# Optimization experiments

Hardware: AMD Instinct MI355X
Metric: run time of the kernel (lower is better)

The kernel has to match this reference:

```python
import jax, jax.numpy as jnp
import numpy as np


def setup_inputs() -> dict:
    key = jax.random.key(0)
    ks = jax.random.split(key, 9)
    B, Nq, Nkv, C, ICO = 1, 512, 2562, 64, 64
    return {
        "q": jax.random.normal(ks[0], (B, Nq, C), jnp.float32),
        "q_coord": jax.random.normal(ks[1], (B, Nq, 3), jnp.float32),
        "kv": jax.random.normal(ks[2], (B, Nkv, ICO), jnp.float32),
        "kv_coord": jax.random.normal(ks[3], (B, Nkv, 3), jnp.float32),
        "Wq": jax.random.normal(ks[4], (C, C), jnp.float32) * (C ** -0.5),
        "Wkv": jax.random.normal(ks[5], (ICO, 2 * C), jnp.float32) * (ICO ** -0.5),
        "Wdelta": jax.random.normal(ks[6], (3, C), jnp.float32) * (3 ** -0.5),
        "Wproj": jax.random.normal(ks[7], (C, C), jnp.float32) * (C ** -0.5),
        "bproj": jnp.zeros((C,), jnp.float32),
    }


def reference(q, q_coord, kv, kv_coord, Wq, Wkv, Wdelta, Wproj, bproj):
    C = q.shape[-1]
    scale = 1.0 / C  # erp_dim ** -1 (qk_scale=None)
    q_ = q @ Wq                                   # [B, Nq, C]
    kv_ = kv @ Wkv                                # [B, Nkv, 2C]
    k, v = jnp.split(kv_, 2, axis=-1)             # each [B, Nkv, C]
    # positional encoding: exp(-|dq - dk|) over 3D coords, projected to C
    pos_enc = jnp.exp(-jnp.abs(q_coord[:, :, None] - kv_coord[:, None])) @ Wdelta  # [B,Nq,Nkv,C]
    # elementwise abs-diff attention score, reduced over channel dim
    score = (jnp.exp(-jnp.abs(q_[:, :, None] - k[:, None])) + pos_enc).sum(-1) * scale  # [B,Nq,Nkv]
    attn = jax.nn.softmax(score, axis=-1)
    out = attn @ v                                # [B, Nq, C]
    return out @ Wproj + bproj
```

## Files before the change

kernel.cpp:

```cpp
#include <hip/hip_runtime.h>

#define NQ   512
#define NKV  2562
#define CH   64
#define QB   4
#define BT   256
#define NJQ  8
#define JQ   321
#define PSTRIDE 260
#define LOG2E 1.44269504088896340736f

#define KVROWS 8
#define NKVB ((NKV + KVROWS - 1) / KVROWS)
#define QROWS 16
#define NQB (NQ / QROWS)
#define NCB  41

static __device__ __forceinline__ float exp2_raw(float x) {
  float r; asm("v_exp_f32 %0, %1" : "=v"(r) : "v"(x)); return r;
}
static __device__ __forceinline__ float exp2_negabs(float x) {
  float r; asm("v_exp_f32 %0, -abs(%1)" : "=v"(r) : "v"(x)); return r;
}
#define E2(a, b) exp2_negabs((a) - (b))
#define T4(qf, kf) ((E2((qf).x, (kf).x) + E2((qf).y, (kf).y)) + \
                    (E2((qf).z, (kf).z) + E2((qf).w, (kf).w)))

__global__ __launch_bounds__(256) void gemm_qkv(
    const float* __restrict__ q, const float* __restrict__ kv,
    const float* __restrict__ Wq, const float* __restrict__ Wkv,
    const float* __restrict__ kvc, float* __restrict__ qp,
    float* __restrict__ kvp, float* __restrict__ kvc4) {
  const int tid = threadIdx.x;
  if (blockIdx.x < NKVB) {
    const int j0 = blockIdx.x * KVROWS;
    __shared__ float s_in[KVROWS][CH];
    if (tid < KVROWS * (CH / 4)) {
      int r = tid >> 4, g = tid & 15;
      int j = j0 + r;
      float4 v = (j < NKV) ? ((const float4*)(kv + (size_t)j * CH))[g]
                           : make_float4(0.f, 0.f, 0.f, 0.f);
      ((float4*)&s_in[r][0])[g] = v;
    }
    __syncthreads();
    const int r = tid >> 5;
    const int mg = (tid & 31) * 4;
    float4 acc = make_float4(0.f, 0.f, 0.f, 0.f);
#pragma unroll 16
    for (int rr = 0; rr < CH; ++rr) {
      float a = s_in[r][rr];
      float4 w = *(const float4*)(Wkv + (size_t)rr * 2 * CH + mg);
      acc.x = fmaf(a, w.x, acc.x); acc.y = fmaf(a, w.y, acc.y);
      acc.z = fmaf(a, w.z, acc.z); acc.w = fmaf(a, w.w, acc.w);
    }
    if (mg < CH) {
      acc.x *= LOG2E; acc.y *= LOG2E; acc.z *= LOG2E; acc.w *= LOG2E;
    }
    int j = j0 + r;
    if (j < NKV) *(float4*)(kvp + (size_t)j * 2 * CH + mg) = acc;
  } else if (blockIdx.x < NKVB + NQB) {
    const int i0 = (blockIdx.x - NKVB) * QROWS;
    __shared__ float s_in[QROWS][CH];
    {
      int r = tid >> 4, g = tid & 15;
      float4 v = ((const float4*)(q + (size_t)(i0 + r) * CH))[g];
      ((float4*)&s_in[r][0])[g] = v;
    }
    __syncthreads();
    const int r = tid >> 4;
    const int cg = (tid & 15) * 4;
    float4 acc = make_float4(0.f, 0.f, 0.f, 0.f);
#pragma unroll 16
    for (int rr = 0; rr < CH; ++rr) {
      float a = s_in[r][rr];
      float4 w = *(const float4*)(Wq + (size_t)rr * CH + cg);
      acc.x = fmaf(a, w.x, acc.x); acc.y = fmaf(a, w.y, acc.y);
      acc.z = fmaf(a, w.z, acc.z); acc.w = fmaf(a, w.w, acc.w);
    }
    acc.x *= LOG2E; acc.y *= LOG2E; acc.z *= LOG2E; acc.w *= LOG2E;
    *(float4*)(qp + (size_t)(i0 + r) * CH + cg) = acc;
  } else {
    int t = (blockIdx.x - NKVB - NQB) * 256 + tid;
    if (t < NKV * 4) {
      int j = t >> 2, d = t & 3;
      kvc4[t] = (d < 3) ? kvc[(size_t)j * 3 + d] * LOG2E : 0.f;
    }
  }
}

__global__ __launch_bounds__(BT, 4) void attn_part(
    const float* __restrict__ qp, const float* __restrict__ kvp,
    const float* __restrict__ qc, const float* __restrict__ kvc4,
    const float* __restrict__ Wdelta, float* __restrict__ part) {
  __shared__ float s_score[QB][JQ];
  __shared__ float s_red[QB][BT];
  __shared__ float s_wd[3];

  const int qquad = blockIdx.x >> 3;
  const int h = blockIdx.x & 7;
  const int i0 = qquad * QB;
  const int jlo = h * JQ;
  const int jhi = (jlo + JQ < NKV) ? jlo + JQ : NKV;

  const int tid = threadIdx.x;
  const int sub = tid & 3;
  const int c0 = sub * 16;
  const int wid = tid >> 6;
  const int lane = tid & 63;

  if (tid < 3) {
    float s = 0.f;
    for (int c = 0; c < CH; ++c) s += Wdelta[tid * CH + c];
    s_wd[tid] = s;
  }

  const float4* pw = (const float4*)(qp + (size_t)(i0 + 0) * CH + c0);
  const float4* px = (const float4*)(qp + (size_t)(i0 + 1) * CH + c0);
  const float4* py = (const float4*)(qp + (size_t)(i0 + 2) * CH + c0);
  const float4* pz = (const float4*)(qp + (size_t)(i0 + 3) * CH + c0);
  float4 qw0 = pw[0], qw1 = pw[1], qw2 = pw[2], qw3 = pw[3];
  float4 qx0 = px[0], qx1 = px[1], qx2 = px[2], qx3 = px[3];
  float4 qy0 = py[0], qy1 = py[1], qy2 = py[2], qy3 = py[3];
  float4 qz0 = pz[0], qz1 = pz[1], qz2 = pz[2], qz3 = pz[3];
  asm volatile("" : "+v"(qw0.x), "+v"(qw0.y), "+v"(qw0.z), "+v"(qw0.w),
                    "+v"(qw1.x), "+v"(qw1.y), "+v"(qw1.z), "+v"(qw1.w),
                    "+v"(qw2.x), "+v"(qw2.y), "+v"(qw2.z), "+v"(qw2.w),
                    "+v"(qw3.x), "+v"(qw3.y), "+v"(qw3.z), "+v"(qw3.w));
  asm volatile("" : "+v"(qx0.x), "+v"(qx0.y), "+v"(qx0.z), "+v"(qx0.w),
                    "+v"(qx1.x), "+v"(qx1.y), "+v"(qx1.z), "+v"(qx1.w),
                    "+v"(qx2.x), "+v"(qx2.y), "+v"(qx2.z), "+v"(qx2.w),
                    "+v"(qx3.x), "+v"(qx3.y), "+v"(qx3.z), "+v"(qx3.w));
  asm volatile("" : "+v"(qy0.x), "+v"(qy0.y), "+v"(qy0.z), "+v"(qy0.w),
                    "+v"(qy1.x), "+v"(qy1.y), "+v"(qy1.z), "+v"(qy1.w),
                    "+v"(qy2.x), "+v"(qy2.y), "+v"(qy2.z), "+v"(qy2.w),
                    "+v"(qy3.x), "+v"(qy3.y), "+v"(qy3.z), "+v"(qy3.w));
  asm volatile("" : "+v"(qz0.x), "+v"(qz0.y), "+v"(qz0.z), "+v"(qz0.w),
                    "+v"(qz1.x), "+v"(qz1.y), "+v"(qz1.z), "+v"(qz1.w),
                    "+v"(qz2.x), "+v"(qz2.y), "+v"(qz2.z), "+v"(qz2.w),
                    "+v"(qz3.x), "+v"(qz3.y), "+v"(qz3.z), "+v"(qz3.w));

  float cw0 = qc[(size_t)(i0 + 0) * 3 + 0] * LOG2E;
  float cw1 = qc[(size_t)(i0 + 0) * 3 + 1] * LOG2E;
  float cw2 = qc[(size_t)(i0 + 0) * 3 + 2] * LOG2E;
  float cx0 = qc[(size_t)(i0 + 1) * 3 + 0] * LOG2E;
  float cx1 = qc[(size_t)(i0 + 1) * 3 + 1] * LOG2E;
  float cx2 = qc[(size_t)(i0 + 1) * 3 + 2] * LOG2E;
  float cy0 = qc[(size_t)(i0 + 2) * 3 + 0] * LOG2E;
  float cy1 = qc[(size_t)(i0 + 2) * 3 + 1] * LOG2E;
  float cy2 = qc[(size_t)(i0 + 2) * 3 + 2] * LOG2E;
  float cz0 = qc[(size_t)(i0 + 3) * 3 + 0] * LOG2E;
  float cz1 = qc[(size_t)(i0 + 3) * 3 + 1] * LOG2E;
  float cz2 = qc[(size_t)(i0 + 3) * 3 + 2] * LOG2E;
  __syncthreads();
  const float wd0 = s_wd[0], wd1 = s_wd[1], wd2 = s_wd[2];
  const float pscale = (1.0f / 64.0f) * LOG2E;

  float lsw = 0.f, lsx = 0.f, lsy = 0.f, lsz = 0.f;
  for (int j = jlo + (tid >> 2); j < jhi; j += BT / 4) {
    const float4* kr = (const float4*)(kvp + (size_t)j * 128 + c0);
    float4 k0 = kr[0], k1 = kr[1], k2 = kr[2], k3 = kr[3];
    float4 cc = *(const float4*)(kvc4 + (size_t)j * 4);

    float sw = (T4(qw0, k0) + T4(qw1, k1)) + (T4(qw2, k2) + T4(qw3, k3));
    float sx = (T4(qx0, k0) + T4(qx1, k1)) + (T4(qx2, k2) + T4(qx3, k3));
    float sy = (T4(qy0, k0) + T4(qy1, k1)) + (T4(qy2, k2) + T4(qy3, k3));
    float sz = (T4(qz0, k0) + T4(qz1, k1)) + (T4(qz2, k2) + T4(qz3, k3));
    sw += __shfl_xor(sw, 1); sw += __shfl_xor(sw, 2);
    sx += __shfl_xor(sx, 1); sx += __shfl_xor(sx, 2);
    sy += __shfl_xor(sy, 1); sy += __shfl_xor(sy, 2);
    sz += __shfl_xor(sz, 1); sz += __shfl_xor(sz, 2);
    if (sub == 0) {
      int jj = j - jlo;
      sw += E2(cw0, cc.x) * wd0 + E2(cw1, cc.y) * wd1 + E2(cw2, cc.z) * wd2;
      sx += E2(cx0, cc.x) * wd0 + E2(cx1, cc.y) * wd1 + E2(cx2, cc.z) * wd2;
      sy += E2(cy0, cc.x) * wd0 + E2(cy1, cc.y) * wd1 + E2(cy2, cc.z) * wd2;
      sz += E2(cz0, cc.x) * wd0 + E2(cz1, cc.y) * wd1 + E2(cz2, cc.z) * wd2;
      float p0 = exp2_raw(sw * pscale);
      float p1 = exp2_raw(sx * pscale);
      float p2 = exp2_raw(sy * pscale);
      float p3 = exp2_raw(sz * pscale);
      s_score[0][jj] = p0; s_score[1][jj] = p1;
      s_score[2][jj] = p2; s_score[3][jj] = p3;
      lsw += p0; lsx += p1; lsy += p2; lsz += p3;
    }
  }

#pragma unroll
  for (int off = 1; off < 64; off <<= 1) {
    lsw += __shfl_xor(lsw, off);
    lsx += __shfl_xor(lsx, off);
    lsy += __shfl_xor(lsy, off);
    lsz += __shfl_xor(lsz, off);
  }
  if (lane == 0) {
    s_red[0][wid] = lsw; s_red[1][wid] = lsx;
    s_red[2][wid] = lsy; s_red[3][wid] = lsz;
  }
  __syncthreads();
  float tw = s_red[0][0], tx = s_red[1][0], ty = s_red[2][0], tz = s_red[3][0];
#pragma unroll
  for (int w = 1; w < BT / 64; ++w) {
    tw += s_red[0][w]; tx += s_red[1][w];
    ty += s_red[2][w]; tz += s_red[3][w];
  }
  __syncthreads();

  const int c = tid & 63, g = tid >> 6;
  float aw = 0.f, ax = 0.f, ay = 0.f, az = 0.f;
#pragma unroll 8
  for (int j2 = jlo + g; j2 < jhi; j2 += 4) {
    float v = kvp[(size_t)j2 * 128 + 64 + c];
    int jj = j2 - jlo;
    aw = fmaf(s_score[0][jj], v, aw);
    ax = fmaf(s_score[1][jj], v, ax);
    ay = fmaf(s_score[2][jj], v, ay);
    az = fmaf(s_score[3][jj], v, az);
  }
  s_red[0][tid] = aw; s_red[1][tid] = ax;
  s_red[2][tid] = ay; s_red[3][tid] = az;
  __syncthreads();

  float* P = part + (size_t)(qquad * NJQ + h) * PSTRIDE;
  if (g == 0) {
    float uw = 0.f, ux = 0.f, uy = 0.f, uz = 0.f;
#pragma unroll
    for (int gg = 0; gg < 4; ++gg) {
      uw += s_red[0][gg * 64 + c];
      ux += s_red[1][gg * 64 + c];
      uy += s_red[2][gg * 64 + c];
      uz += s_red[3][gg * 64 + c];
    }
    P[4 + 0 * 64 + c] = uw;
    P[4 + 1 * 64 + c] = ux;
    P[4 + 2 * 64 + c] = uy;
    P[4 + 3 * 64 + c] = uz;
    if (c == 0) { P[0] = tw; P[1] = tx; P[2] = ty; P[3] = tz; }
  }
}

__global__ __launch_bounds__(256) void attn_merge(
    const float* __restrict__ part, const float* __restrict__ Wproj,
    const float* __restrict__ bproj, float* __restrict__ out) {
  __shared__ float s_o[4][CH];
  const int tid = threadIdx.x;
  const int qs = tid >> 6, c = tid & 63;
  const int qquad = blockIdx.x;
  const int i = qquad * 4 + qs;

  float ssum = 0.f, osum = 0.f;
#pragma unroll
  for (int h = 0; h < NJQ; ++h) {
    const float* P = part + (size_t)(qquad * NJQ + h) * PSTRIDE;
    ssum += P[qs];
    osum += P[4 + qs * 64 + c];
  }
  s_o[qs][c] = osum / ssum;
  __syncthreads();

  float acc = 0.f;
#pragma unroll 16
  for (int r = 0; r < CH; ++r)
    acc = fmaf(s_o[qs][r], Wproj[r * CH + c], acc);
  out[(size_t)i * CH + c] = acc + bproj[c];
}

extern "C" void kernel_launch(void* const* d_in, const int* in_sizes, int n_in,
                              void* d_out, int out_size, void* d_ws, size_t ws_size,
                              hipStream_t stream) {
  const float* q      = (const float*)d_in[0];
  const float* qc     = (const float*)d_in[1];
  const float* kv     = (const float*)d_in[2];
  const float* kvc    = (const float*)d_in[3];
  const float* Wq     = (const float*)d_in[4];
  const float* Wkv    = (const float*)d_in[5];
  const float* Wdelta = (const float*)d_in[6];
  const float* Wproj  = (const float*)d_in[7];
  const float* bproj  = (const float*)d_in[8];
  float* outp = (float*)d_out;

  float* qp   = (float*)d_ws;
  float* kvp  = qp + NQ * CH;
  float* part = kvp + (size_t)NKV * 2 * CH;
  float* kvc4 = part + (size_t)(NQ / QB) * NJQ * PSTRIDE;

  gemm_qkv<<<NKVB + NQB + NCB, 256, 0, stream>>>(q, kv, Wq, Wkv, kvc, qp, kvp, kvc4);
  attn_part<<<(NQ / QB) * NJQ, BT, 0, stream>>>(qp, kvp, qc, kvc4, Wdelta, part);
  attn_merge<<<NQ / QB, 256, 0, stream>>>(part, Wproj, bproj, outp);
}
```

Measured before the change: 102.8 us.

## Fuse merge kernel into attn_part via last-block atomic counter

Removes the separate attn_merge launch. Each attn_part block bumps a per-query-quad atomic counter after writing its partial results, and the last of the eight blocks reads all partials, normalises them and applies the output projection. The counters are zeroed inside gemm_qkv. This saves one kernel launch and its gap, at the cost of thread fences, an atomic per block and a serial tail inside the final block of each group.

```diff
diff --git a/kernel.cpp b/kernel.cpp
--- a/kernel.cpp
+++ b/kernel.cpp
@@ -30,7 +30,8 @@
     const float* __restrict__ q, const float* __restrict__ kv,
     const float* __restrict__ Wq, const float* __restrict__ Wkv,
     const float* __restrict__ kvc, float* __restrict__ qp,
-    float* __restrict__ kvp, float* __restrict__ kvc4) {
+    float* __restrict__ kvp, float* __restrict__ kvc4,
+    int* __restrict__ counters) {
   const int tid = threadIdx.x;
   if (blockIdx.x < NKVB) {
     const int j0 = blockIdx.x * KVROWS;
@@ -80,7 +81,9 @@
     acc.x *= LOG2E; acc.y *= LOG2E; acc.z *= LOG2E; acc.w *= LOG2E;
     *(float4*)(qp + (size_t)(i0 + r) * CH + cg) = acc;
   } else {
-    int t = (blockIdx.x - NKVB - NQB) * 256 + tid;
+    int b = blockIdx.x - NKVB - NQB;
+    if (b == 0 && tid < NQ / QB) counters[tid] = 0;
+    int t = b * 256 + tid;
     if (t < NKV * 4) {
       int j = t >> 2, d = t & 3;
       kvc4[t] = (d < 3) ? kvc[(size_t)j * 3 + d] * LOG2E : 0.f;
@@ -91,10 +94,13 @@
 __global__ __launch_bounds__(BT, 4) void attn_part(
     const float* __restrict__ qp, const float* __restrict__ kvp,
     const float* __restrict__ qc, const float* __restrict__ kvc4,
-    const float* __restrict__ Wdelta, float* __restrict__ part) {
+    const float* __restrict__ Wdelta, float* __restrict__ part,
+    int* __restrict__ counters, const float* __restrict__ Wproj,
+    const float* __restrict__ bproj, float* __restrict__ out) {
   __shared__ float s_score[QB][JQ];
   __shared__ float s_red[QB][BT];
   __shared__ float s_wd[3];
+  __shared__ int s_last;
 
   const int qquad = blockIdx.x >> 3;
   const int h = blockIdx.x & 7;
@@ -236,32 +242,31 @@
     P[4 + 3 * 64 + c] = uz;
     if (c == 0) { P[0] = tw; P[1] = tx; P[2] = ty; P[3] = tz; }
   }
-}
-
-__global__ __launch_bounds__(256) void attn_merge(
-    const float* __restrict__ part, const float* __restrict__ Wproj,
-    const float* __restrict__ bproj, float* __restrict__ out) {
-  __shared__ float s_o[4][CH];
-  const int tid = threadIdx.x;
-  const int qs = tid >> 6, c = tid & 63;
-  const int qquad = blockIdx.x;
-  const int i = qquad * 4 + qs;
-
+
+  __threadfence();
+  if (tid == 0) {
+    int old = atomicAdd(&counters[qquad], 1);
+    s_last = (old == NJQ - 1) ? 1 : 0;
+  }
+  __syncthreads();
+  if (!s_last) return;
+  __threadfence();
+
+  const int qs = tid >> 6;
   float ssum = 0.f, osum = 0.f;
 #pragma unroll
-  for (int h = 0; h < NJQ; ++h) {
-    const float* P = part + (size_t)(qquad * NJQ + h) * PSTRIDE;
-    ssum += P[qs];
-    osum += P[4 + qs * 64 + c];
-  }
-  s_o[qs][c] = osum / ssum;
-  __syncthreads();
-
+  for (int hh = 0; hh < NJQ; ++hh) {
+    const float* Pm = part + (size_t)(qquad * NJQ + hh) * PSTRIDE;
+    ssum += Pm[qs];
+    osum += Pm[4 + qs * 64 + c];
+  }
+  s_red[0][tid] = osum / ssum;
+  __syncthreads();
   float acc = 0.f;
 #pragma unroll 16
   for (int r = 0; r < CH; ++r)
-    acc = fmaf(s_o[qs][r], Wproj[r * CH + c], acc);
-  out[(size_t)i * CH + c] = acc + bproj[c];
+    acc = fmaf(s_red[0][(tid & ~63) + r], Wproj[r * CH + c], acc);
+  out[(size_t)(i0 + qs) * CH + c] = acc + bproj[c];
 }
 
 extern "C" void kernel_launch(void* const* d_in, const int* in_sizes, int n_in,
@@ -282,8 +287,10 @@
   float* kvp  = qp + NQ * CH;
   float* part = kvp + (size_t)NKV * 2 * CH;
   float* kvc4 = part + (size_t)(NQ / QB) * NJQ * PSTRIDE;
-
-  gemm_qkv<<<NKVB + NQB + NCB, 256, 0, stream>>>(q, kv, Wq, Wkv, kvc, qp, kvp, kvc4);
-  attn_part<<<(NQ / QB) * NJQ, BT, 0, stream>>>(qp, kvp, qc, kvc4, Wdelta, part);
-  attn_merge<<<NQ / QB, 256, 0, stream>>>(part, Wproj, bproj, outp);
-}
+  int* counters = (int*)(kvc4 + (size_t)NKV * 4);
+
+  gemm_qkv<<<NKVB + NQB + NCB, 256, 0, stream>>>(q, kv, Wq, Wkv, kvc, qp, kvp,
+                                                 kvc4, counters);
+  attn_part<<<(NQ / QB) * NJQ, BT, 0, stream>>>(qp, kvp, qc, kvc4, Wdelta, part,
+                                                counters, Wproj, bproj, outp);
+}
```

Result: slower. 198.2 us (+92.8%).
